# Optimization experiments

Hardware: AMD Instinct MI355X
Metric: run time of the kernel (lower is better)

## Reference

```python
import jax, jax.numpy as jnp
import numpy as np

L, H, T, G, B, F = 4, 512, 128, 16, 64, 64  # layers, hidden, seq, group, batch, features


def setup_inputs() -> dict:
    key = jax.random.key(0)
    ks = jax.random.split(key, 13)
    s = 0.02
    return {
        "input_window": jax.random.normal(ks[0], (B, T, F), jnp.float32),
        "W": jax.random.normal(ks[1], (L, 5 * H, H), jnp.float32) * s,
        "Z": jax.random.normal(ks[2], (L, 5 * H, H), jnp.float32) * s,
        "U": jax.random.normal(ks[3], (L, 5 * H, H + G), jnp.float32) * s,
        "V": jax.random.normal(ks[4], (L, 5 * H, H), jnp.float32) * s,
        "J": jax.random.normal(ks[5], (L, 5 * H, G), jnp.float32) * s,
        "b": jnp.zeros((L, 5 * H), jnp.float32),
        "boundary": jax.random.uniform(ks[6], (L, T), jnp.float32),
        "Q": jax.random.normal(ks[7], (L, L * H, H), jnp.float32) * s,
        "R": jax.random.normal(ks[8], (L, H, H), jnp.float32) * s,
        "Wo": jax.random.normal(ks[9], (F, H), jnp.float32) * s,
        "bo": jnp.zeros((F,), jnp.float32),
    }


def _forward(input_window, W, Z, U, V, J, b, boundary, Q, R, Wo, bo):
    dt = input_window.dtype
    mask = ~jnp.isnan(input_window)
    x = jnp.nan_to_num(input_window, nan=0.0)
    bt = (boundary > 0.5).astype(dt)                      # [L,T] step(initial_boundary)
    # contiguous feature groups -> reshape; [T,L,B,G]
    x_g = x.reshape(B, T, L, G).transpose(1, 2, 0, 3)
    z_g = jnp.any(mask.reshape(B, T, L, G), axis=-1)[..., None].transpose(1, 2, 0, 3)  # [T,L,B,1] bool

    def step(carry, inp):
        h_prev, c_prev, s_prev = carry                    # [L,B,H],[L,B,H],[L]
        xg_t, z_t, b_t = inp                              # [L,B,G],[L,B,1],[L]
        h_list, c_list = [], []
        s_list = [b_t[k] for k in range(L)]
        for k in range(L):
            kp, kn = max(k - 1, 0), min(k + 1, L - 1)
            h_low = jnp.zeros((B, H), dt) if k == 0 else h_list[k - 1]   # h_curr[k_prev]
            lower = s_list[kp]
            prev = s_prev[k]
            p_hi, l_hi = prev >= 0.5, lower >= 0.5
            m1 = ((~p_hi) & l_hi).astype(dt)
            m2 = (p_hi & (~l_hi)).astype(dt)
            m3 = (p_hi & l_hi).astype(dt)
            m4 = ((~p_hi) & (~l_hi)).astype(dt)
            aW = h_prev[k] @ W[k].T                        # [B,5H]
            aZ = h_prev[kn] @ Z[k].T
            aU = jnp.concatenate([h_low, xg_t[k]], axis=1) @ U[k].T
            aV = h_low @ V[k].T
            aJ = xg_t[k] @ J[k].T
            t2 = jnp.where(z_t[k], aU, aV)
            t2J = jnp.where(z_t[k], aJ, jnp.zeros_like(aJ))
            pre = b[k] + m1 * (aW + t2) + m2 * (aZ + t2J) + m3 * (aZ + t2)
            pre_f = b[k][:H] + m1 * (aW[:, :H] + t2[:, :H])            # forget: only op1
            f = jax.nn.sigmoid(pre_f)
            g = jnp.tanh(pre[:, H:2 * H])
            i = jax.nn.sigmoid(pre[:, 2 * H:3 * H])
            o = jax.nn.sigmoid(pre[:, 3 * H:4 * H])
            sg = jnp.clip((pre[:, 4 * H:5 * H] + 1.0) / 2.0, 0.0, 1.0)
            s_list[k] = (jnp.mean(sg) > 0.5).astype(dt)
            c_new = m1 * (f * c_prev[k] + i * g) + (m2 + m3) * (i * g) + m4 * c_prev[k]
            h_new = m4 * (o * jnp.tanh(c_new)) + (1.0 - m4) * h_prev[k]
            h_list.append(h_new)
            c_list.append(c_new)
        h_c = jnp.stack(h_list)
        return (h_c, jnp.stack(c_list), jnp.stack(s_list)), h_c

    zero = jnp.zeros((L, B, H), dt)
    (_, h_hist) = jax.lax.scan(step, (zero, zero, bt[:, 0]), (x_g, z_g, bt.T))[0:2] if False else jax.lax.scan(step, (zero, zero, bt[:, 0]), (x_g, z_g, bt.T))
    h = h_hist.transpose(1, 2, 0, 3)                      # [L,B,T,H]
    # HierarchicalStateExcitation
    h_bg = h.transpose(1, 0, 2, 3)                        # [B,L,T,H]
    h_cat = h_bg.transpose(0, 2, 1, 3).reshape(B, T, L * H)
    r = jax.nn.sigmoid(jnp.einsum('btf,kfh->bkth', h_cat, Q))
    mul1 = jnp.einsum('bkth,khg->bktg', r, R)
    excited = jax.nn.relu(jnp.sum(mul1 * h_bg, axis=1))   # [B,T,H]
    return excited @ Wo.T + bo                            # [B,T,F]


def reference(input_window, W, Z, U, V, J, b, boundary, Q, R, Wo, bo):
    return _forward(input_window, W, Z, U, V, J, b, boundary, Q, R, Wo, bo)
```

## Files before the change

### kernel.cpp

```cpp
#include <hip/hip_runtime.h>
#include <hip/hip_bf16.h>


#define LL 4
#define HH 512
#define TS 128
#define GG 16
#define BB 64
#define FF 64
#define FIVE_H 2560
#define LBH (LL * BB * HH)

typedef unsigned short u16;
typedef unsigned int u32;
typedef unsigned long long u64;

typedef short bfrag8 __attribute__((ext_vector_type(8)));
typedef float facc4 __attribute__((ext_vector_type(4)));

#define SG_OFF    64
#define ZALL_OFF  1024
#define ZMASK_OFF 2048
#define C_OFF     4096
#define PING_OFF  (C_OFF + LBH)
#define PART_OFF  (PING_OFF + 2 * LBH)
#define PART_SEG  (12 * 4 * HH * BB)
#define HIST_OFF  (PART_OFF + 2 * PART_SEG)
#define HFRAG_OFF (HIST_OFF + 8388608)
#define WFRAG_OFF (HFRAG_OFF + 262144)
#define EXC_OFF   (HIST_OFF + 4194304)

__device__ __forceinline__ float bf2f(u16 u) { return __uint_as_float(((u32)u) << 16); }
__device__ __forceinline__ float2 bf2x2(u32 u) {
    float2 r;
    r.x = __uint_as_float(u << 16);
    r.y = __uint_as_float(u & 0xFFFF0000u);
    return r;
}
__device__ __forceinline__ u16 f2bf_rne(float f) {
    u32 x = __float_as_uint(f);
    return (u16)((x + 0x7FFFu + ((x >> 16) & 1u)) >> 16);
}
__device__ __forceinline__ float sigm(float x) { return 1.f / (1.f + expf(-x)); }

template <bool BF>
__device__ __forceinline__ float ldv(const void* p, size_t i) {
    return BF ? bf2f(((const u16*)p)[i]) : ((const float*)p)[i];
}

template <bool BF>
__device__ __forceinline__ float dot16(const void* row, const float* xs) {
    float s = 0.f;
    if (BF) {
        const uint4* p = (const uint4*)row;
        uint4 a = p[0], b4 = p[1];
        float2 v;
        v = bf2x2(a.x);  s += v.x * xs[0]  + v.y * xs[1];
        v = bf2x2(a.y);  s += v.x * xs[2]  + v.y * xs[3];
        v = bf2x2(a.z);  s += v.x * xs[4]  + v.y * xs[5];
        v = bf2x2(a.w);  s += v.x * xs[6]  + v.y * xs[7];
        v = bf2x2(b4.x); s += v.x * xs[8]  + v.y * xs[9];
        v = bf2x2(b4.y); s += v.x * xs[10] + v.y * xs[11];
        v = bf2x2(b4.z); s += v.x * xs[12] + v.y * xs[13];
        v = bf2x2(b4.w); s += v.x * xs[14] + v.y * xs[15];
    } else {
        const float4* p = (const float4*)row;
#pragma unroll
        for (int i = 0; i < 4; ++i) {
            float4 v = p[i];
            s += v.x * xs[4 * i] + v.y * xs[4 * i + 1] + v.z * xs[4 * i + 2] + v.w * xs[4 * i + 3];
        }
    }
    return s;
}

__global__ void initA_kernel(const u16* __restrict__ bnd_raw, float* __restrict__ ws) {
    size_t i = (size_t)blockIdx.x * 256 + threadIdx.x;
    if (i < LBH) ws[C_OFF + i] = 0.f;
    if (i < 512) ws[SG_OFF + i] = 0.f;
    if (i == 0) {
        int bf = 1;
        for (int j = 0; j < 32; ++j) {
            float v = bf2f(bnd_raw[2 * j]);
            if (!(v >= 0.f && v <= 1.f)) bf = 0;
        }
        ((int*)ws)[0] = bf;
    }
}

template <bool BF>
__device__ void initB_body(const void* xin, float* ws) {
    int tk = blockIdx.x;
    int t = tk >> 2, k = tk & 3;
    int b = threadIdx.x;
    bool z = false;
    size_t base = (size_t)b * TS * FF + (size_t)t * FF + k * GG;
#pragma unroll
    for (int g = 0; g < GG; ++g) {
        float v = ldv<BF>(xin, base + g);
        z |= !(v != v);
    }
    u64 m = __ballot(z);
    if (b == 0) {
        ((u64*)(ws + ZMASK_OFF))[tk] = m;
        ((int*)(ws + ZALL_OFF))[tk] = (m == ~0ull) ? 1 : 0;
    }
}
__global__ __launch_bounds__(64) void initB_kernel(const void* xin, float* ws) {
    int mode = ((const int*)ws)[0];
    if (mode) initB_body<true>(xin, ws);
    else      initB_body<false>(xin, ws);
}

__global__ __launch_bounds__(256) void prep_kernel(
    const void* Wm, const void* Zm, const void* Um, const void* Vm, float* ws) {
    if (((const int*)ws)[0] == 0) return;
    int gw = (int)((blockIdx.x * 256 + threadIdx.x) >> 6);
    int lane = threadIdx.x & 63;
    int ml = gw / 2560, r = gw - ml * 2560;
    int mi = ml >> 2, k = ml & 3;
    int RS = (mi == 2) ? (HH + GG) : HH;
    const void* M = (mi == 0) ? Wm : (mi == 1) ? Zm : (mi == 2) ? Um : Vm;
    const u16* src = (const u16*)M + (size_t)k * FIVE_H * RS + (size_t)r * RS + lane * 8;
    uint4 v = *(const uint4*)src;
    int q = lane >> 4, kb = (lane >> 2) & 3, qd = lane & 3;
    int slab = r >> 6, wv = (r >> 4) & 3, m = r & 15;
    u16* dst = (u16*)(ws + WFRAG_OFF) + (size_t)ml * (2560 * 512)
             + ((((size_t)(slab * 4 + q) * 4 + wv) * 4 + kb) * 64 + (qd * 16 + m)) * 8;
    *(uint4*)dst = v;
}

template <bool BF>
__device__ __forceinline__ void phase_meta(const void* bnd, const float* ws,
                                           int tau, int s,
                                           int& t, int& k, int& mcase, int& azf, int& nblk) {
    k = (tau & 1) + 2 * s;
    t = (tau - k) >> 1;
    mcase = 4; azf = 0; nblk = 0;
    if (t < 0 || t >= TS) { t = -1; return; }
    const float* sgsum = ws + SG_OFF;
    bool p_hi = (t == 0) ? (ldv<BF>(bnd, (size_t)k * TS) > 0.5f) : (sgsum[(t - 1) * 4 + k] > 16384.f);
    bool l_hi = (k == 0) ? (ldv<BF>(bnd, (size_t)t) > 0.5f) : (sgsum[t * 4 + (k - 1)] > 16384.f);
    mcase = p_hi ? (l_hi ? 3 : 2) : (l_hi ? 1 : 4);
    azf = ((const int*)(ws + ZALL_OFF))[t * 4 + k] ? 0 : 1;
    if (mcase == 4) return;
    int gs = (mcase == 1) ? 0 : 1, ng = 4 - gs;
    int nW = (t > 0) ? ng : 0;
    int nU = ((mcase == 1 || mcase == 3) && k > 0) ? ng : 0;
    int nV = azf ? nU : 0;
    nblk = (nW + nU + nV) * 32;
}

struct SlotInfo {
    const u16* M16; const float* Mf; int RS; int path; int g;
    const float* hv;
};
template <bool BF>
__device__ __forceinline__ SlotInfo slot_info(
    const void* Wm, const void* Zm, const void* Um, const void* Vm,
    const float* ws, int unit, int t, int k, int mcase) {
    int gs = (mcase == 1) ? 0 : 1, ng = 4 - gs;
    int nW = (t > 0) ? ng : 0;
    int nU = ((mcase == 1 || mcase == 3) && k > 0) ? ng : 0;
    int mat, g;
    if (unit < nW)            { mat = (mcase == 1) ? 0 : 1; g = gs + unit; }
    else if (unit < nW + nU)  { mat = 2; g = gs + unit - nW; }
    else                      { mat = 3; g = gs + unit - nW - nU; }
    const void* M = (mat == 0) ? Wm : (mat == 1) ? Zm : (mat == 2) ? Um : Vm;
    int kn = (k + 1 < LL) ? k + 1 : LL - 1;
    const float* ping = ws + PING_OFF;
    const float* prev = ping + (size_t)((t + 1) & 1) * LBH;
    const float* cur  = ping + (size_t)(t & 1) * LBH;
    SlotInfo si;
    si.M16 = (const u16*)M; si.Mf = (const float*)M;
    si.RS = (mat == 2) ? (HH + GG) : HH;
    si.path = (mat <= 1) ? 0 : (mat == 2 ? 1 : 2);
    si.g = g;
    si.hv = (mat == 0) ? prev + (size_t)k * HH * BB
          : (mat == 1) ? prev + (size_t)kn * HH * BB
                       : cur + (size_t)(k - 1) * HH * BB;
    return si;
}

__device__ void gemm_slot_bf(float* ws, int seg, int idx, int t, int k, int mcase) {
    int tid = threadIdx.x;
    int q = idx & 3, sub = (idx >> 2) & 7, unit = idx >> 5;
    int gs = (mcase == 1) ? 0 : 1, ng = 4 - gs;
    int nW = (t > 0) ? ng : 0;
    int nU = ((mcase == 1 || mcase == 3) && k > 0) ? ng : 0;
    int mat, g;
    if (unit < nW)            { mat = (mcase == 1) ? 0 : 1; g = gs + unit; }
    else if (unit < nW + nU)  { mat = 2; g = gs + unit - nW; }
    else                      { mat = 3; g = gs + unit - nW - nU; }
    int path = (mat <= 1) ? 0 : (mat == 2 ? 1 : 2);
    int slab = (g < 3) ? g * 8 + sub : 32 + sub;

    int lb, par;
    if (mat == 0)      { lb = k;  par = (t + 1) & 1; }
    else if (mat == 1) { lb = (k + 1 < LL) ? k + 1 : LL - 1; par = (t + 1) & 1; }
    else               { lb = k - 1; par = t & 1; }

    int lane = tid & 63, wave = tid >> 6;
    int m = lane & 15, qd = lane >> 4;

    const u16* af = (const u16*)(ws + WFRAG_OFF)
                  + (size_t)(mat * 4 + k) * (2560 * 512)
                  + (size_t)(slab * 4 + q) * 8192 + wave * 2048 + lane * 8;
    const u16* hf = (const u16*)(ws + HFRAG_OFF) + (size_t)((par * 4 + lb) * 2) * 32768;

    facc4 acc[4];
#pragma unroll
    for (int i = 0; i < 4; ++i) acc[i] = (facc4){0.f, 0.f, 0.f, 0.f};
#pragma unroll
    for (int kb = 0; kb < 4; ++kb) {
        bfrag8 a = *(const bfrag8*)(af + kb * 512);
        size_t hbk = (size_t)(q * 16 + kb * 4 + qd) * 512 + m * 8;
#pragma unroll
        for (int bg = 0; bg < 4; ++bg) {
            bfrag8 bh = *(const bfrag8*)(hf + hbk + bg * 128);
            bfrag8 bl = *(const bfrag8*)(hf + 32768 + hbk + bg * 128);
            acc[bg] = __builtin_amdgcn_mfma_f32_16x16x32_bf16(a, bh, acc[bg], 0, 0, 0);
            acc[bg] = __builtin_amdgcn_mfma_f32_16x16x32_bf16(a, bl, acc[bg], 0, 0, 0);
        }
    }
    float* pout = ws + PART_OFF + (size_t)seg * PART_SEG +
                  ((size_t)(path * 4 + q) * 4 + g) * (size_t)HH * BB;
#pragma unroll
    for (int bg = 0; bg < 4; ++bg)
#pragma unroll
        for (int reg = 0; reg < 4; ++reg)
            pout[(size_t)(sub * 64 + wave * 16 + qd * 4 + reg) * BB + bg * 16 + m] = acc[bg][reg];
}

__device__ void gemm_slot_f32(const void* Wm, const void* Zm, const void* Um, const void* Vm,
                              float* ws, float* wt, float* ht,
                              int seg, int idx, int t, int k, int mcase) {
    int tid = threadIdx.x;
    int q = idx & 3, sub = (idx >> 2) & 7, unit = idx >> 5;
    SlotInfo si = slot_info<false>(Wm, Zm, Um, Vm, ws, unit, t, k, mcase);
    int gbase = (si.g < 3) ? si.g * 512 : 2048;
    size_t mbase = (size_t)k * FIVE_H * si.RS + (size_t)(gbase + sub * 64) * si.RS + q * 128;

    int rg = tid >> 4, bg = tid & 15;
    float acc[4][4] = {{0.f}};
    for (int half = 0; half < 2; ++half) {
        int sr = tid >> 2, scg = (tid & 3) * 16;
        size_t rowoff = mbase + (size_t)sr * si.RS + half * 64 + scg;
#pragma unroll
        for (int i = 0; i < 4; ++i)
            *(float4*)&wt[sr * 68 + scg + 4 * i] = *(const float4*)(si.Mf + rowoff + 4 * i);
        int hc = tid >> 2, hb = (tid & 3) * 16;
        const float* hrow = si.hv + (size_t)(q * 128 + half * 64 + hc) * BB + hb;
#pragma unroll
        for (int i = 0; i < 4; ++i)
            *(float4*)&ht[hc * 68 + hb + 4 * i] = *(const float4*)(hrow + 4 * i);
        __syncthreads();
#pragma unroll 4
        for (int kk4 = 0; kk4 < 64; kk4 += 4) {
            float w[4][4], h[4][4];
#pragma unroll
            for (int j = 0; j < 4; ++j)
                *(float4*)w[j] = *(const float4*)&wt[(rg * 4 + j) * 68 + kk4];
#pragma unroll
            for (int j = 0; j < 4; ++j)
                *(float4*)h[j] = *(const float4*)&ht[(kk4 + j) * 68 + bg * 4];
#pragma unroll
            for (int rj = 0; rj < 4; ++rj)
#pragma unroll
                for (int bj = 0; bj < 4; ++bj)
#pragma unroll
                    for (int j = 0; j < 4; ++j)
                        acc[rj][bj] += w[rj][j] * h[j][bj];
        }
        __syncthreads();
    }
    float* pout = ws + PART_OFF + (size_t)seg * PART_SEG +
                  ((size_t)(si.path * 4 + q) * 4 + si.g) * (size_t)HH * BB;
#pragma unroll
    for (int rj = 0; rj < 4; ++rj) {
        float4 vv = make_float4(acc[rj][0], acc[rj][1], acc[rj][2], acc[rj][3]);
        *(float4*)&pout[(size_t)(sub * 64 + rg * 4 + rj) * BB + bg * 4] = vv;
    }
}

__global__ __launch_bounds__(256) void gemm_phase_kernel(
    const void* Wm, const void* Zm, const void* Um, const void* Vm,
    const void* bnd, float* ws, int tau) {
    __shared__ __align__(16) u16 gsm[26112];
    int mode = ((const int*)ws)[0];
    if (mode) {
        int t0, k0, m0, a0, n0, t1, k1, m1, a1, n1;
        phase_meta<true>(bnd, ws, tau, 0, t0, k0, m0, a0, n0);
        phase_meta<true>(bnd, ws, tau, 1, t1, k1, m1, a1, n1);
        int bid = blockIdx.x;
        if (bid < n0)           gemm_slot_bf(ws, 0, bid, t0, k0, m0);
        else if (bid < n0 + n1) gemm_slot_bf(ws, 1, bid - n0, t1, k1, m1);
    } else {
        float* fs = (float*)gsm;
        int t0, k0, m0, a0, n0, t1, k1, m1, a1, n1;
        phase_meta<false>(bnd, ws, tau, 0, t0, k0, m0, a0, n0);
        phase_meta<false>(bnd, ws, tau, 1, t1, k1, m1, a1, n1);
        int bid = blockIdx.x;
        if (bid < n0)           gemm_slot_f32(Wm, Zm, Um, Vm, ws, fs, fs + 4352, 0, bid, t0, k0, m0);
        else if (bid < n0 + n1) gemm_slot_f32(Wm, Zm, Um, Vm, ws, fs, fs + 4352, 1, bid - n0, t1, k1, m1);
    }
}

template <bool BF>
__device__ void gates_slot(const void* xin, const void* Um, const void* Jm,
                           const void* bbias, float* ws, float* smem,
                           int seg, int jblk, int t, int k, int mcase, int azf) {
    float (*xs)[GG + 1] = (float (*)[GG + 1])smem;
    float* red = smem + BB * (GG + 1);
    int tid = threadIdx.x;
    int j = jblk * 4 + (tid >> 6);
    int b = tid & 63;

    {
        int b2 = tid >> 2, i0 = (tid & 3) * 4;
#pragma unroll
        for (int i = 0; i < 4; ++i) {
            float v = ldv<BF>(xin, (size_t)b2 * TS * FF + (size_t)t * FF + k * GG + i0 + i);
            xs[b2][i0 + i] = (v != v) ? 0.f : v;
        }
    }
    __syncthreads();
    u64 zm = ((const u64*)(ws + ZMASK_OFF))[t * 4 + k];
    bool zb = (zm >> b) & 1ull;

    float* cbuf = ws + C_OFF;
    const float* part = ws + PART_OFF + (size_t)seg * PART_SEG;
    float* cur = ws + PING_OFF + (size_t)(t & 1) * LBH;
    const float* prev = ws + PING_OFF + (size_t)((t + 1) & 1) * LBH;
    u16* hist = (u16*)(ws + HIST_OFF);
    size_t sidx = ((size_t)k * HH + j) * BB + b;

    float hn, sgv;
    if (mcase == 4) {
        float c = cbuf[sidx];
        float o = sigm(ldv<BF>(bbias, (size_t)k * FIVE_H + 1536 + j));
        hn = o * tanhf(c);
        float bsg = ldv<BF>(bbias, (size_t)k * FIVE_H + 2048 + j);
        sgv = fminf(fmaxf((bsg + 1.f) * 0.5f, 0.f), 1.f);
    } else {
        bool hasWZ = (t > 0);
        bool hasU = (k > 0) && (mcase != 2);
        const float* xv = &xs[b][0];
        auto psum = [&](int path, int g) -> float {
            float s = 0.f;
#pragma unroll
            for (int qq = 0; qq < 4; ++qq)
                s += part[(((size_t)(path * 4 + qq) * 4 + g) * HH + j) * BB + b];
            return s;
        };
        auto pre = [&](int g) -> float {
            int gb = (g < 3) ? g * 512 : 2048;
            float s = ldv<BF>(bbias, (size_t)k * FIVE_H + gb + j);
            if (hasWZ) s += psum(0, g);
            if (mcase == 2) {
                if (zb) {
                    const void* row = BF ? (const void*)((const u16*)Jm + (size_t)k * FIVE_H * GG + (size_t)(gb + j) * GG)
                                         : (const void*)((const float*)Jm + (size_t)k * FIVE_H * GG + (size_t)(gb + j) * GG);
                    s += dot16<BF>(row, xv);
                }
            } else {
                if (zb) {
                    if (hasU) s += psum(1, g);
                    const void* row = BF ? (const void*)((const u16*)Um + (size_t)k * FIVE_H * (HH + GG) + (size_t)(gb + j) * (HH + GG) + HH)
                                         : (const void*)((const float*)Um + (size_t)k * FIVE_H * (HH + GG) + (size_t)(gb + j) * (HH + GG) + HH);
                    s += dot16<BF>(row, xv);
                } else {
                    if (hasU && azf) s += psum(2, g);
                }
            }
            return s;
        };
        float preg = pre(1), prei = pre(2), presg = pre(3);
        float gg = tanhf(preg), ii = sigm(prei);
        float cnew;
        if (mcase == 1) {
            float f = sigm(pre(0));
            cnew = f * cbuf[sidx] + ii * gg;
        } else {
            cnew = ii * gg;
        }
        cbuf[sidx] = cnew;
        hn = (t > 0) ? prev[sidx] : 0.f;
        sgv = fminf(fmaxf((presg + 1.f) * 0.5f, 0.f), 1.f);
    }
    cur[sidx] = hn;
    u16 hi = f2bf_rne(hn);
    hist[((size_t)(t * 4 + k) * HH + j) * BB + b] = hi;
    if (BF) {
        u16 lo = f2bf_rne(hn - bf2f(hi));
        u16* hfw = (u16*)(ws + HFRAG_OFF) + (size_t)(((t & 1) * 4 + k) * 2) * 32768;
        size_t fo = ((size_t)(j >> 3) * 64 + b) * 8 + (j & 7);
        hfw[fo] = hi;
        hfw[32768 + fo] = lo;
    }

    float s = sgv;
#pragma unroll
    for (int off = 32; off > 0; off >>= 1) s += __shfl_down(s, off);
    if ((tid & 63) == 0) red[tid >> 6] = s;
    __syncthreads();
    if (tid == 0)
        atomicAdd(&ws[SG_OFF + t * 4 + k], red[0] + red[1] + red[2] + red[3]);
}

template <bool BF>
__device__ void gates_phase_body(const void* xin, const void* Um, const void* Jm,
                                 const void* bbias, const void* bnd, float* ws,
                                 float* smem, int tau) {
    int seg = blockIdx.x >> 7, jblk = blockIdx.x & 127;
    int t, k, mc, az, nb;
    phase_meta<BF>(bnd, ws, tau, seg, t, k, mc, az, nb);
    if (t >= 0)
        gates_slot<BF>(xin, Um, Jm, bbias, ws, smem, seg, jblk, t, k, mc, az);
}
__global__ __launch_bounds__(256) void gates_phase_kernel(
    const void* xin, const void* Um, const void* Jm, const void* bbias,
    const void* bnd, float* ws, int tau) {
    __shared__ float smem[BB * (GG + 1) + 4];
    int mode = ((const int*)ws)[0];
    if (mode) gates_phase_body<true>(xin, Um, Jm, bbias, bnd, ws, smem, tau);
    else      gates_phase_body<false>(xin, Um, Jm, bbias, bnd, ws, smem, tau);
}

template <bool BF>
__device__ void fragprep_body(const void* src, float* ws, int Fext, int which) {
    int tid = threadIdx.x;
    int nfg = Fext >> 6;
    int gc = blockIdx.x & 3;
    int bo = blockIdx.x >> 2;
    int ko = bo / nfg, fg = bo % nfg;
    size_t kstride = (size_t)Fext * 512;
    u16 *dhi, *dlo;
    if (which == 0) { dhi = (u16*)(ws + WFRAG_OFF) + 16777216; dlo = (u16*)(ws + PART_OFF); }
    else            { dhi = (u16*)(ws + PART_OFF) + 4194304;   dlo = dhi + 1048576; }
    __shared__ float S[64][129];
    for (int it = 0; it < 32; ++it) {
        int idx = it * 256 + tid;
        int f = idx >> 7, n = idx & 127;
        S[f][n] = ldv<BF>(src, ko * kstride + (size_t)(fg * 64 + f) * 512 + gc * 128 + n);
    }
    __syncthreads();
    for (int it = 0; it < 4; ++it) {
        int idx = it * 256 + tid;
        int fbl = idx >> 7, n = idx & 127;
        u32 hiw[4], low[4];
#pragma unroll
        for (int jp = 0; jp < 4; ++jp) {
            float v0 = S[fbl * 8 + 2 * jp][n], v1 = S[fbl * 8 + 2 * jp + 1][n];
            u16 h0 = f2bf_rne(v0), h1 = f2bf_rne(v1);
            u16 l0 = f2bf_rne(v0 - bf2f(h0)), l1 = f2bf_rne(v1 - bf2f(h1));
            hiw[jp] = (u32)h0 | ((u32)h1 << 16);
            low[jp] = (u32)l0 | ((u32)l1 << 16);
        }
        size_t o = (((size_t)ko * (Fext >> 3) + fg * 8 + fbl) * 512 + gc * 128 + n) * 8;
        *(uint4*)(dhi + o) = make_uint4(hiw[0], hiw[1], hiw[2], hiw[3]);
        *(uint4*)(dlo + o) = make_uint4(low[0], low[1], low[2], low[3]);
    }
}
__global__ __launch_bounds__(256) void fragprep_kernel(const void* src, float* ws,
                                                       int Fext, int which) {
    int mode = ((const int*)ws)[0];
    if (mode) fragprep_body<true>(src, ws, Fext, which);
    else      fragprep_body<false>(src, ws, Fext, which);
}

__global__ __launch_bounds__(256) void transpose_kernel(float* ws) {
    int tk = blockIdx.x;
    int t = tk >> 2, k = tk & 3;
    const u16* hist = (const u16*)(ws + HIST_OFF);
    u16* hT = (u16*)(ws + WFRAG_OFF);
    __shared__ u16 T[64][72];
    int tid = threadIdx.x;
    for (int j0 = 0; j0 < 512; j0 += 64) {
        int jl = tid >> 3, b0 = (tid & 7) * 8;
        *(uint4*)&T[jl][b0]      = *(const uint4*)&hist[((size_t)tk * 512 + j0 + jl) * 64 + b0];
        *(uint4*)&T[jl + 32][b0] = *(const uint4*)&hist[((size_t)tk * 512 + j0 + jl + 32) * 64 + b0];
        __syncthreads();
        int b = tid >> 2, jj0 = (tid & 3) * 16;
        u16 tmp[16];
#pragma unroll
        for (int i = 0; i < 16; ++i) tmp[i] = T[jj0 + i][b];
        u16* dst = &hT[((size_t)(b * 128 + t)) * 2048 + k * 512 + j0 + jj0];
        *(uint4*)&dst[0] = *(uint4*)&tmp[0];
        *(uint4*)&dst[8] = *(uint4*)&tmp[8];
        __syncthreads();
    }
}

__global__ __launch_bounds__(256) void exciteR_kernel(float* ws, int k) {
    int tid = threadIdx.x, lane = tid & 63, w = tid >> 6;
    int m = lane & 15, qd = lane >> 4;
    int bb = blockIdx.x >> 3, oct = blockIdx.x & 7;
    int h0 = oct * 64;
    const u16* hT = (const u16*)(ws + WFRAG_OFF);
    const u16* qhi = hT + 16777216;
    const u16* qlo = (const u16*)(ws + PART_OFF);
    const u16* A = hT + (size_t)(bb * 128 + w * 32) * 2048;

    facc4 acc[2][4];
#pragma unroll
    for (int i = 0; i < 2; ++i)
#pragma unroll
        for (int j = 0; j < 4; ++j) acc[i][j] = (facc4){0.f, 0.f, 0.f, 0.f};

    for (int kc = 0; kc < 64; ++kc) {
        bfrag8 a0 = *(const bfrag8*)(A + (size_t)m * 2048 + kc * 32 + qd * 8);
        bfrag8 a1 = *(const bfrag8*)(A + (size_t)(16 + m) * 2048 + kc * 32 + qd * 8);
        size_t qb = ((size_t)(k * 256 + kc * 4 + qd) * 512 + h0 + m) * 8;
#pragma unroll
        for (int nt = 0; nt < 4; ++nt) {
            bfrag8 bh = *(const bfrag8*)(qhi + qb + nt * 128);
            bfrag8 bl = *(const bfrag8*)(qlo + qb + nt * 128);
            acc[0][nt] = __builtin_amdgcn_mfma_f32_16x16x32_bf16(a0, bh, acc[0][nt], 0, 0, 0);
            acc[0][nt] = __builtin_amdgcn_mfma_f32_16x16x32_bf16(a0, bl, acc[0][nt], 0, 0, 0);
            acc[1][nt] = __builtin_amdgcn_mfma_f32_16x16x32_bf16(a1, bh, acc[1][nt], 0, 0, 0);
            acc[1][nt] = __builtin_amdgcn_mfma_f32_16x16x32_bf16(a1, bl, acc[1][nt], 0, 0, 0);
        }
    }
    u16* rhi = (u16*)(ws + HIST_OFF);
    u16* rlo = rhi + 4194304;
#pragma unroll
    for (int mt = 0; mt < 2; ++mt)
#pragma unroll
        for (int nt = 0; nt < 4; ++nt)
#pragma unroll
            for (int reg = 0; reg < 4; ++reg) {
                float rv = sigm(acc[mt][nt][reg]);
                int t = w * 32 + mt * 16 + qd * 4 + reg;
                int h = h0 + nt * 16 + m;
                size_t o = (size_t)(bb * 128 + t) * 512 + h;
                u16 hi = f2bf_rne(rv);
                rhi[o] = hi;
                rlo[o] = f2bf_rne(rv - bf2f(hi));
            }
}

__global__ __launch_bounds__(256) void exciteM_kernel(float* ws, int k) {
    int tid = threadIdx.x, lane = tid & 63, w = tid >> 6;
    int m = lane & 15, qd = lane >> 4;
    int bb = blockIdx.x >> 3, tt = (blockIdx.x >> 1) & 3, gh = blockIdx.x & 1;
    int g0 = gh * 256 + w * 64;
    const u16* rhi = (const u16*)(ws + HIST_OFF);
    const u16* rlo = rhi + 4194304;
    const u16* rfhi = (const u16*)(ws + PART_OFF) + 4194304;
    const u16* rflo = rfhi + 1048576;
    const u16* Ahi = rhi + (size_t)(bb * 128 + tt * 32) * 512;
    const u16* Alo = rlo + (size_t)(bb * 128 + tt * 32) * 512;

    facc4 acc[2][4];
#pragma unroll
    for (int i = 0; i < 2; ++i)
#pragma unroll
        for (int j = 0; j < 4; ++j) acc[i][j] = (facc4){0.f, 0.f, 0.f, 0.f};

    for (int kc = 0; kc < 16; ++kc) {
        bfrag8 ah0 = *(const bfrag8*)(Ahi + (size_t)m * 512 + kc * 32 + qd * 8);
        bfrag8 ah1 = *(const bfrag8*)(Ahi + (size_t)(16 + m) * 512 + kc * 32 + qd * 8);
        bfrag8 al0 = *(const bfrag8*)(Alo + (size_t)m * 512 + kc * 32 + qd * 8);
        bfrag8 al1 = *(const bfrag8*)(Alo + (size_t)(16 + m) * 512 + kc * 32 + qd * 8);
        size_t rb = ((size_t)(k * 64 + kc * 4 + qd) * 512 + g0 + m) * 8;
#pragma unroll
        for (int nt = 0; nt < 4; ++nt) {
            bfrag8 bh = *(const bfrag8*)(rfhi + rb + nt * 128);
            bfrag8 bl = *(const bfrag8*)(rflo + rb + nt * 128);
            acc[0][nt] = __builtin_amdgcn_mfma_f32_16x16x32_bf16(ah0, bh, acc[0][nt], 0, 0, 0);
            acc[0][nt] = __builtin_amdgcn_mfma_f32_16x16x32_bf16(ah0, bl, acc[0][nt], 0, 0, 0);
            acc[0][nt] = __builtin_amdgcn_mfma_f32_16x16x32_bf16(al0, bh, acc[0][nt], 0, 0, 0);
            acc[1][nt] = __builtin_amdgcn_mfma_f32_16x16x32_bf16(ah1, bh, acc[1][nt], 0, 0, 0);
            acc[1][nt] = __builtin_amdgcn_mfma_f32_16x16x32_bf16(ah1, bl, acc[1][nt], 0, 0, 0);
            acc[1][nt] = __builtin_amdgcn_mfma_f32_16x16x32_bf16(al1, bh, acc[1][nt], 0, 0, 0);
        }
    }
    const u16* hT = (const u16*)(ws + WFRAG_OFF);
    float* exc = ws + EXC_OFF;
#pragma unroll
    for (int mt = 0; mt < 2; ++mt)
#pragma unroll
        for (int nt = 0; nt < 4; ++nt)
#pragma unroll
            for (int reg = 0; reg < 4; ++reg) {
                int t = tt * 32 + mt * 16 + qd * 4 + reg;
                int g = g0 + nt * 16 + m;
                float hv = bf2f(hT[(size_t)(bb * 128 + t) * 2048 + k * 512 + g]);
                size_t o = (size_t)(bb * 128 + t) * 512 + g;
                float v = acc[mt][nt][reg] * hv;
                if (k == 0) exc[o] = v;
                else        exc[o] += v;
            }
}

__global__ __launch_bounds__(256) void exciteO_kernel(
    const float* ws, const void* Wom, const void* bom, void* out) {
    int mode = ((const int*)ws)[0];
    __shared__ float S[8][512];
    int bb = blockIdx.x >> 4, tg = blockIdx.x & 15;
    const float* exc = ws + EXC_OFF + ((size_t)(bb * 128 + tg * 8)) * 512;
    int tid = threadIdx.x;
    for (int it = 0; it < 16; ++it) {
        int idx = it * 256 + tid;
        int tl = idx >> 9, g = idx & 511;
        S[tl][g] = fmaxf(exc[(size_t)tl * 512 + g], 0.f);
    }
    __syncthreads();
    int fo = tid & 63, tl0 = tid >> 6;
#pragma unroll
    for (int rep = 0; rep < 2; ++rep) {
        int tl = tl0 + rep * 4;
        float acc = 0.f;
        if (mode) {
            const uint4* wp = (const uint4*)((const u16*)Wom + (size_t)fo * HH);
            const float4* ev = (const float4*)S[tl];
#pragma unroll 8
            for (int it = 0; it < HH / 8; ++it) {
                uint4 qv = wp[it];
                float4 e0 = ev[2 * it], e1 = ev[2 * it + 1];
                float2 a0 = bf2x2(qv.x), a1 = bf2x2(qv.y), a2 = bf2x2(qv.z), a3 = bf2x2(qv.w);
                acc += a0.x * e0.x + a0.y * e0.y + a1.x * e0.z + a1.y * e0.w +
                       a2.x * e1.x + a2.y * e1.y + a3.x * e1.z + a3.y * e1.w;
            }
        } else {
            const float4* wp = (const float4*)((const float*)Wom + (size_t)fo * HH);
            const float4* ev = (const float4*)S[tl];
#pragma unroll 8
            for (int it = 0; it < HH / 4; ++it) {
                float4 qv = wp[it], e = ev[it];
                acc += qv.x * e.x + qv.y * e.y + qv.z * e.z + qv.w * e.w;
            }
        }
        acc += mode ? bf2f(((const u16*)bom)[fo]) : ((const float*)bom)[fo];
        int t = tg * 8 + tl;
        size_t oidx = ((size_t)bb * TS + t) * FF + fo;
        if (mode) ((u16*)out)[oidx] = f2bf_rne(acc);
        else      ((float*)out)[oidx] = acc;
    }
}

extern "C" void kernel_launch(void* const* d_in, const int* in_sizes, int n_in,
                              void* d_out, int out_size, void* d_ws, size_t ws_size,
                              hipStream_t stream) {
    const void* xin = d_in[0];
    const void* Wm  = d_in[1];
    const void* Zm  = d_in[2];
    const void* Um  = d_in[3];
    const void* Vm  = d_in[4];
    const void* Jm  = d_in[5];
    const void* bb  = d_in[6];
    const void* bnd = d_in[7];
    const void* Qm  = d_in[8];
    const void* Rm  = d_in[9];
    const void* Wo  = d_in[10];
    const void* bo  = d_in[11];
    float* ws = (float*)d_ws;

    initA_kernel<<<dim3(512), dim3(256), 0, stream>>>((const u16*)bnd, ws);
    initB_kernel<<<dim3(512), dim3(64), 0, stream>>>(xin, ws);
    prep_kernel<<<dim3(10240), dim3(256), 0, stream>>>(Wm, Zm, Um, Vm, ws);
    for (int tau = 0; tau < 2 * TS + LL - 2; ++tau) {
        gemm_phase_kernel<<<dim3(768), dim3(256), 0, stream>>>(Wm, Zm, Um, Vm, bnd, ws, tau);
        gates_phase_kernel<<<dim3(256), dim3(256), 0, stream>>>(xin, Um, Jm, bb, bnd, ws, tau);
    }
    fragprep_kernel<<<dim3(512), dim3(256), 0, stream>>>(Qm, ws, 2048, 0);
    fragprep_kernel<<<dim3(128), dim3(256), 0, stream>>>(Rm, ws, 512, 1);
    transpose_kernel<<<dim3(512), dim3(256), 0, stream>>>(ws);
    for (int k = 0; k < LL; ++k) {
        exciteR_kernel<<<dim3(512), dim3(256), 0, stream>>>(ws, k);
        exciteM_kernel<<<dim3(512), dim3(256), 0, stream>>>(ws, k);
    }
    exciteO_kernel<<<dim3(1024), dim3(256), 0, stream>>>(ws, Wo, bo, d_out);
}
```

Before: 4.663 ms.

## Fuse per-step GEMM and gates kernels with atomic counter handoff

```diff
diff --git a/kernel.cpp b/kernel.cpp
--- a/kernel.cpp
+++ b/kernel.cpp
@@ -28,6 +28,7 @@
 #define HIST_OFF  (PART_OFF + 2 * PART_SEG)
 #define HFRAG_OFF (HIST_OFF + 8388608)
 #define WFRAG_OFF (HFRAG_OFF + 262144)
+#define CNT_OFF   (WFRAG_OFF + 10485760)
 #define EXC_OFF   (HIST_OFF + 4194304)
 
 __device__ __forceinline__ float bf2f(u16 u) { return __uint_as_float(((u32)u) << 16); }
@@ -42,6 +43,17 @@
     return (u16)((x + 0x7FFFu + ((x >> 16) & 1u)) >> 16);
 }
 __device__ __forceinline__ float sigm(float x) { return 1.f / (1.f + expf(-x)); }
+
+__device__ __forceinline__ void st_agent(float* p, float v) {
+    __hip_atomic_store(p, v, __ATOMIC_RELAXED, __HIP_MEMORY_SCOPE_AGENT);
+}
+__device__ __forceinline__ void st_agent2(float* p, float a, float b) {
+    u64 v = ((u64)__float_as_uint(b) << 32) | (u64)__float_as_uint(a);
+    __hip_atomic_store((u64*)p, v, __ATOMIC_RELAXED, __HIP_MEMORY_SCOPE_AGENT);
+}
+__device__ __forceinline__ float ld_agent(const float* p) {
+    return __hip_atomic_load((float*)p, __ATOMIC_RELAXED, __HIP_MEMORY_SCOPE_AGENT);
+}
 
 template <bool BF>
 __device__ __forceinline__ float ldv(const void* p, size_t i) {
@@ -78,6 +90,7 @@
     size_t i = (size_t)blockIdx.x * 256 + threadIdx.x;
     if (i < LBH) ws[C_OFF + i] = 0.f;
     if (i < 512) ws[SG_OFF + i] = 0.f;
+    if (i < 258 * 32) ((int*)(ws + CNT_OFF))[i] = 0;
     if (i == 0) {
         int bf = 1;
         for (int j = 0; j < 32; ++j) {
@@ -229,7 +242,8 @@
     for (int bg = 0; bg < 4; ++bg)
 #pragma unroll
         for (int reg = 0; reg < 4; ++reg)
-            pout[(size_t)(sub * 64 + wave * 16 + qd * 4 + reg) * BB + bg * 16 + m] = acc[bg][reg];
+            st_agent(&pout[(size_t)(sub * 64 + wave * 16 + qd * 4 + reg) * BB + bg * 16 + m],
+                     acc[bg][reg]);
 }
 
 __device__ void gemm_slot_f32(const void* Wm, const void* Zm, const void* Um, const void* Vm,
@@ -278,38 +292,17 @@
                   ((size_t)(si.path * 4 + q) * 4 + si.g) * (size_t)HH * BB;
 #pragma unroll
     for (int rj = 0; rj < 4; ++rj) {
-        float4 vv = make_float4(acc[rj][0], acc[rj][1], acc[rj][2], acc[rj][3]);
-        *(float4*)&pout[(size_t)(sub * 64 + rg * 4 + rj) * BB + bg * 4] = vv;
-    }
-}
-
-__global__ __launch_bounds__(256) void gemm_phase_kernel(
-    const void* Wm, const void* Zm, const void* Um, const void* Vm,
-    const void* bnd, float* ws, int tau) {
-    __shared__ __align__(16) u16 gsm[26112];
-    int mode = ((const int*)ws)[0];
-    if (mode) {
-        int t0, k0, m0, a0, n0, t1, k1, m1, a1, n1;
-        phase_meta<true>(bnd, ws, tau, 0, t0, k0, m0, a0, n0);
-        phase_meta<true>(bnd, ws, tau, 1, t1, k1, m1, a1, n1);
-        int bid = blockIdx.x;
-        if (bid < n0)           gemm_slot_bf(ws, 0, bid, t0, k0, m0);
-        else if (bid < n0 + n1) gemm_slot_bf(ws, 1, bid - n0, t1, k1, m1);
-    } else {
-        float* fs = (float*)gsm;
-        int t0, k0, m0, a0, n0, t1, k1, m1, a1, n1;
-        phase_meta<false>(bnd, ws, tau, 0, t0, k0, m0, a0, n0);
-        phase_meta<false>(bnd, ws, tau, 1, t1, k1, m1, a1, n1);
-        int bid = blockIdx.x;
-        if (bid < n0)           gemm_slot_f32(Wm, Zm, Um, Vm, ws, fs, fs + 4352, 0, bid, t0, k0, m0);
-        else if (bid < n0 + n1) gemm_slot_f32(Wm, Zm, Um, Vm, ws, fs, fs + 4352, 1, bid - n0, t1, k1, m1);
+        float* p = &pout[(size_t)(sub * 64 + rg * 4 + rj) * BB + bg * 4];
+        st_agent2(p, acc[rj][0], acc[rj][1]);
+        st_agent2(p + 2, acc[rj][2], acc[rj][3]);
     }
 }
 
 template <bool BF>
 __device__ void gates_slot(const void* xin, const void* Um, const void* Jm,
                            const void* bbias, float* ws, float* smem,
-                           int seg, int jblk, int t, int k, int mcase, int azf) {
+                           int seg, int jblk, int t, int k, int mcase, int azf,
+                           int* wcnt, int tgt) {
     float (*xs)[GG + 1] = (float (*)[GG + 1])smem;
     float* red = smem + BB * (GG + 1);
     int tid = threadIdx.x;
@@ -325,6 +318,13 @@
         }
     }
     __syncthreads();
+    if (wcnt && tgt > 0) {
+        if (tid == 0) {
+            while (__hip_atomic_load(wcnt, __ATOMIC_RELAXED, __HIP_MEMORY_SCOPE_AGENT) < tgt)
+                __builtin_amdgcn_s_sleep(1);
+        }
+        __syncthreads();
+    }
     u64 zm = ((const u64*)(ws + ZMASK_OFF))[t * 4 + k];
     bool zb = (zm >> b) & 1ull;
 
@@ -350,7 +350,7 @@
             float s = 0.f;
 #pragma unroll
             for (int qq = 0; qq < 4; ++qq)
-                s += part[(((size_t)(path * 4 + qq) * 4 + g) * HH + j) * BB + b];
+                s += ld_agent(&part[(((size_t)(path * 4 + qq) * 4 + g) * HH + j) * BB + b]);
             return s;
         };
         auto pre = [&](int g) -> float {
@@ -408,23 +408,49 @@
         atomicAdd(&ws[SG_OFF + t * 4 + k], red[0] + red[1] + red[2] + red[3]);
 }
 
-template <bool BF>
-__device__ void gates_phase_body(const void* xin, const void* Um, const void* Jm,
-                                 const void* bbias, const void* bnd, float* ws,
-                                 float* smem, int tau) {
-    int seg = blockIdx.x >> 7, jblk = blockIdx.x & 127;
-    int t, k, mc, az, nb;
-    phase_meta<BF>(bnd, ws, tau, seg, t, k, mc, az, nb);
-    if (t >= 0)
-        gates_slot<BF>(xin, Um, Jm, bbias, ws, smem, seg, jblk, t, k, mc, az);
-}
-__global__ __launch_bounds__(256) void gates_phase_kernel(
-    const void* xin, const void* Um, const void* Jm, const void* bbias,
+__global__ __launch_bounds__(256) void phase_kernel(
+    const void* Wm, const void* Zm, const void* Um, const void* Vm,
+    const void* xin, const void* Jm, const void* bbias,
     const void* bnd, float* ws, int tau) {
-    __shared__ float smem[BB * (GG + 1) + 4];
+    __shared__ __align__(16) float fs[8708];
     int mode = ((const int*)ws)[0];
-    if (mode) gates_phase_body<true>(xin, Um, Jm, bbias, bnd, ws, smem, tau);
-    else      gates_phase_body<false>(xin, Um, Jm, bbias, bnd, ws, smem, tau);
+    int t0, k0, m0, a0, n0, t1, k1, m1, a1, n1;
+    if (mode) {
+        phase_meta<true>(bnd, ws, tau, 0, t0, k0, m0, a0, n0);
+        phase_meta<true>(bnd, ws, tau, 1, t1, k1, m1, a1, n1);
+    } else {
+        phase_meta<false>(bnd, ws, tau, 0, t0, k0, m0, a0, n0);
+        phase_meta<false>(bnd, ws, tau, 1, t1, k1, m1, a1, n1);
+    }
+    int bid = blockIdx.x, tid = threadIdx.x;
+    int* cnt = (int*)(ws + CNT_OFF) + tau * 32;
+
+    if (bid < 768) {
+        int ntot = n0 + n1;
+        if (bid >= ntot) return;
+        if (mode) {
+            if (bid < n0) gemm_slot_bf(ws, 0, bid, t0, k0, m0);
+            else          gemm_slot_bf(ws, 1, bid - n0, t1, k1, m1);
+        } else {
+            if (bid < n0) gemm_slot_f32(Wm, Zm, Um, Vm, ws, fs, fs + 4352, 0, bid, t0, k0, m0);
+            else          gemm_slot_f32(Wm, Zm, Um, Vm, ws, fs, fs + 4352, 1, bid - n0, t1, k1, m1);
+        }
+        __syncthreads();
+        if (tid == 0) {
+            int unit = bid >> 5;
+            if (atomicAdd(&cnt[2 + unit], 1) == 31)
+                atomicAdd(&cnt[(bid < n0) ? 0 : 1], 1);
+        }
+    } else {
+        int gid = bid - 768;
+        int seg = gid >> 7, jblk = gid & 127;
+        int t = seg ? t1 : t0, k = seg ? k1 : k0;
+        int mc = seg ? m1 : m0, az = seg ? a1 : a0;
+        int tgt = (seg ? n1 : n0) >> 5;
+        if (t < 0) return;
+        if (mode) gates_slot<true>(xin, Um, Jm, bbias, ws, fs, seg, jblk, t, k, mc, az, &cnt[seg], tgt);
+        else      gates_slot<false>(xin, Um, Jm, bbias, ws, fs, seg, jblk, t, k, mc, az, &cnt[seg], tgt);
+    }
 }
 
 template <bool BF>
@@ -661,8 +687,8 @@
     initB_kernel<<<dim3(512), dim3(64), 0, stream>>>(xin, ws);
     prep_kernel<<<dim3(10240), dim3(256), 0, stream>>>(Wm, Zm, Um, Vm, ws);
     for (int tau = 0; tau < 2 * TS + LL - 2; ++tau) {
-        gemm_phase_kernel<<<dim3(768), dim3(256), 0, stream>>>(Wm, Zm, Um, Vm, bnd, ws, tau);
-        gates_phase_kernel<<<dim3(256), dim3(256), 0, stream>>>(xin, Um, Jm, bb, bnd, ws, tau);
+        phase_kernel<<<dim3(1024), dim3(256), 0, stream>>>(
+            Wm, Zm, Um, Vm, xin, Jm, bb, bnd, ws, tau);
     }
     fragprep_kernel<<<dim3(512), dim3(256), 0, stream>>>(Qm, ws, 2048, 0);
     fragprep_kernel<<<dim3(128), dim3(256), 0, stream>>>(Rm, ws, 512, 1);
```

New measurement: 7.257 ms. +55.6%, slower.
